# Optimization experiments

Hardware: AMD Instinct MI355X
Metric: run time of the kernel (lower is better)

The kernel has to match this reference:

```python
import jax, jax.numpy as jnp
import numpy as np
from jax.scipy.special import gammaln

# NQ_IN + 4 == 2*H is required because the two kernel=1, padding=1 convs grow the
# length axis by 4 and the following nn.Linear(2H, H) acts on the length axis.
B, NQ_IN, NK, QDIM, KDIM, H = 16, 2044, 1024, 80, 256, 1024


def setup_inputs() -> dict:
    ks = jax.random.split(jax.random.key(0), 14)
    s = 0.02
    return {
        "query": jax.random.normal(ks[0], (B, NQ_IN, QDIM), jnp.float32),
        "key": jax.random.normal(ks[1], (B, NK, KDIM), jnp.float32),
        "query_lens": jnp.full((B,), 2 * H, jnp.int32),
        "key_lens": jnp.full((B,), NK, jnp.int32),
        # query branch params (Conv1d k=1 stored as (out,in); Linear as (out,in))
        "qc1_w": jax.random.normal(ks[2], (2 * H, QDIM), jnp.float32) * s,
        "qc1_b": jax.random.normal(ks[3], (2 * H,), jnp.float32) * s,
        "qc2_w": jax.random.normal(ks[4], (2 * H, 2 * H), jnp.float32) * s,
        "qc2_b": jax.random.normal(ks[5], (2 * H,), jnp.float32) * s,
        "ql_w": jax.random.normal(ks[6], (H, 2 * H), jnp.float32) * s,
        "ql_b": jax.random.normal(ks[7], (H,), jnp.float32) * s,
        # key branch params
        "kc_w": jax.random.normal(ks[8], (H, KDIM, 3), jnp.float32) * s,
        "kc_b": jax.random.normal(ks[9], (H,), jnp.float32) * s,
        "kl1_w": jax.random.normal(ks[10], (2 * H, H), jnp.float32) * s,
        "kl1_b": jax.random.normal(ks[11], (2 * H,), jnp.float32) * s,
        "kl2_w": jax.random.normal(ks[12], (H, 2 * H), jnp.float32) * s,
        "kl2_b": jax.random.normal(ks[13], (H,), jnp.float32) * s,
    }


def _log_beta_binom(query_lens, key_lens, tq, tk):
    # Standard MAS beta-binomial alignment prior over a (tq, tk) grid.
    i = jnp.arange(tq, dtype=jnp.float32)[None, :, None]
    j = jnp.arange(tk, dtype=jnp.float32)[None, None, :]
    ql = query_lens.astype(jnp.float32)[:, None, None]
    kl = key_lens.astype(jnp.float32)[:, None, None]
    a = i + 1.0
    b = jnp.maximum(ql - i, 1.0)
    n = jnp.maximum(kl - 1.0, 0.0)
    nmj = jnp.maximum(n - j, 0.0)

    def betaln(x, y):
        return gammaln(x) + gammaln(y) - gammaln(x + y)

    logp = (gammaln(n + 1.0) - gammaln(j + 1.0) - gammaln(nmj + 1.0)
            + betaln(j + a, nmj + b) - betaln(a, b))
    valid = (i < ql) & (j < kl)
    return jnp.where(valid, logp, -1e9)


def _forward(query, key, query_lens, key_lens,
             qc1_w, qc1_b, qc2_w, qc2_b, ql_w, ql_b,
             kc_w, kc_b, kl1_w, kl1_b, kl2_w, kl2_b):
    # query branch: b n c -> b c n, two k=1/p=1 convs (pad length, pointwise), Linear over LENGTH axis
    q = jnp.transpose(query, (0, 2, 1))                       # (B, QDIM, NQ_IN)
    q = jnp.pad(q, ((0, 0), (0, 0), (1, 1)))
    q = jnp.einsum('bcn,oc->bon', q, qc1_w) + qc1_b[None, :, None]   # (B, 2H, NQ_IN+2)
    q = jnp.pad(q, ((0, 0), (0, 0), (1, 1)))
    q = jnp.einsum('bcn,oc->bon', q, qc2_w) + qc2_b[None, :, None]   # (B, 2H, 2H)
    q = jnp.einsum('bcn,hn->bch', q, ql_w) + ql_b                    # (B, 2H, H) Linear on length axis

    # key branch: b n c -> b c n, Conv1d k=3 p=1, then two Linears over LENGTH axis
    k = jnp.transpose(key, (0, 2, 1))                         # (B, KDIM, NK)
    k = jax.lax.conv_general_dilated(k, kc_w, (1,), ((1, 1),),
                                     dimension_numbers=('NCH', 'OIH', 'NCH'))
    k = k + kc_b[None, :, None]                               # (B, H, NK=H)
    k = jnp.einsum('bcn,on->bco', k, kl1_w) + kl1_b           # (B, H, 2H)
    k = jnp.einsum('bco,ho->bch', k, kl2_w) + kl2_b           # (B, H, H)

    # dist = -cdist(q, k), computed via the GEMM form (same as torch.cdist mm mode)
    sq = (jnp.sum(q * q, -1)[:, :, None] + jnp.sum(k * k, -1)[:, None, :]
          - 2.0 * jnp.einsum('bnd,bmd->bnm', q, k))           # (B, 2H, H)
    dist = -jnp.sqrt(jnp.maximum(sq, 1e-12))

    prior = _log_beta_binom(query_lens, key_lens, q.shape[1], k.shape[1])
    return jax.nn.log_softmax(dist + prior, axis=-1)


def reference(query, key, query_lens, key_lens,
              qc1_w, qc1_b, qc2_w, qc2_b, ql_w, ql_b,
              kc_w, kc_b, kl1_w, kl1_b, kl2_w, kl2_b):
    return _forward(query, key, query_lens, key_lens,
                    qc1_w, qc1_b, qc2_w, qc2_b, ql_w, ql_b,
                    kc_w, kc_b, kl1_w, kl1_b, kl2_w, kl2_b)
```

## Files before the change

### kernel.cpp

```cpp
#include <hip/hip_runtime.h>
#include <math.h>

typedef unsigned short u16;
typedef float floatx4 __attribute__((ext_vector_type(4)));
typedef __bf16 bf16x8 __attribute__((ext_vector_type(8)));

#define BB   16
#define TQ   2048
#define TK   1024
#define HH   1024
#define H2   2048
#define QD   80
#define QDP  128
#define KD   256
#define NQ   2044
#define NKEY 1024

__device__ __forceinline__ u16 f2bf(float f) {
  unsigned int u = __float_as_uint(f);
  u = u + 0x7fffu + ((u >> 16) & 1u);
  return (u16)(u >> 16);
}
__device__ __forceinline__ float bf2f(u16 s) {
  return __uint_as_float(((unsigned int)s) << 16);
}

__global__ __launch_bounds__(256) void prep_all_k(
    const float* __restrict__ qc2_w, const float* __restrict__ kl2_w,
    const float* __restrict__ ql_w, const float* __restrict__ kc_w,
    const float* __restrict__ kl1_w,
    u16* __restrict__ qc2w, u16* __restrict__ kl2w, u16* __restrict__ qlw2,
    u16* __restrict__ kcp, float* __restrict__ colsum1, float* __restrict__ tbl)
{
  long b = blockIdx.x;
  const int t = threadIdx.x;
  __shared__ float red[256];
  if (b < 16384) {
    long i = b * 256 + t; qc2w[i] = f2bf(qc2_w[i]); return;
  }
  b -= 16384;
  if (b < 8192) {
    long i = b * 256 + t; kl2w[i] = f2bf(kl2_w[i]); return;
  }
  b -= 8192;
  if (b < 8192) {
    long i = b * 256 + t;
    int n = (int)(i & 2047);
    int h = (int)(i >> 11);
    qlw2[i] = (n < NQ) ? f2bf(ql_w[(long)h * H2 + n + 2]) : (u16)0; return;
  }
  b -= 8192;
  if (b < 3072) {
    long i = b * 256 + t;
    int r = (int)(i % 768);
    int o = (int)(i / 768);
    int tt = r >> 8, d = r & 255;
    kcp[i] = f2bf(kc_w[((long)o * KD + d) * 3 + tt]); return;
  }
  b -= 3072;
  if (b < 2048) {
    const float* row = kl1_w + b * (long)HH;
    float s = row[t] + row[t + 256] + row[t + 512] + row[t + 768];
    red[t] = s; __syncthreads();
    for (int st = 128; st > 0; st >>= 1) { if (t < st) red[t] += red[t + st]; __syncthreads(); }
    if (!t) colsum1[b] = red[0];
    return;
  }
  b -= 2048;
  { int i = (int)(b * 256 + t); if (i < 8192) tbl[i] = i ? (float)lgamma((double)i) : 0.0f; }
}

__global__ __launch_bounds__(256) void tpack_k(
    const float* __restrict__ kl1_w, const float* __restrict__ qc1_w,
    const float* __restrict__ query,
    u16* __restrict__ kl1T, u16* __restrict__ qc1T, u16* __restrict__ qT)
{
  __shared__ float tile[64][65];
  int bid = blockIdx.x;
  const int tid = threadIdx.x;
  const int r4 = tid >> 6, c = tid & 63;
  const float* src; u16* dst;
  int sr0, sc0, srcR, srcC, srcStride, dstC;
  if (bid < 512) {
    sr0 = (bid >> 4) * 64; sc0 = (bid & 15) * 64;
    src = kl1_w; srcR = 2048; srcC = 1024; srcStride = 1024;
    dst = kl1T; dstC = 2048;
  } else if ((bid -= 512) < 64) {
    sr0 = (bid >> 1) * 64; sc0 = (bid & 1) * 64;
    src = qc1_w; srcR = 2048; srcC = QD; srcStride = QD;
    dst = qc1T; dstC = 2048;
  } else {
    bid -= 64;
    const int b16 = bid >> 6, r = bid & 63;
    sr0 = (r >> 1) * 64; sc0 = (r & 1) * 64;
    src = query + (long)b16 * NQ * QD; srcR = NQ; srcC = QD; srcStride = QD;
    dst = qT + (long)b16 * QDP * 2048; dstC = 2048;
  }
#pragma unroll
  for (int rr = r4; rr < 64; rr += 4) {
    const int gr = sr0 + rr, gc = sc0 + c;
    tile[rr][c] = (gr < srcR && gc < srcC) ? src[(long)gr * srcStride + gc] : 0.f;
  }
  __syncthreads();
#pragma unroll
  for (int rr = r4; rr < 64; rr += 4)
    dst[(long)(sc0 + rr) * dstC + sr0 + c] = f2bf(tile[c][rr]);
}

__global__ __launch_bounds__(256) void pack_kcolT_k(const float* __restrict__ key, u16* __restrict__ out) {
  __shared__ float tile[64][65];
  const int bid = blockIdx.x, tid = threadIdx.x;
  const int b = bid >> 6, r = bid & 63;
  const int m0 = (r >> 2) * 64;
  const int d0 = (r & 3) * 64;
  const int r4 = tid >> 6, c = tid & 63;
#pragma unroll
  for (int rr = r4; rr < 64; rr += 4)
    tile[rr][c] = key[((long)b * NKEY + m0 + rr) * KD + d0 + c];
  __syncthreads();
#pragma unroll
  for (int t = 0; t < 3; t++) {
    const int n = m0 + 1 - t + c;
    if (n >= 0 && n < NKEY) {
#pragma unroll
      for (int rr = r4; rr < 64; rr += 4)
        out[((long)b * 768 + t * 256 + d0 + rr) * NKEY + n] = f2bf(tile[c][rr]);
    }
  }
  if (m0 == 0 && c == 0) {
#pragma unroll
    for (int rr = r4; rr < 64; rr += 4)
      out[((long)b * 768 + d0 + rr) * NKEY + 0] = (u16)0;
  }
  if (m0 == 960 && c == 0) {
#pragma unroll
    for (int rr = r4; rr < 64; rr += 4)
      out[((long)b * 768 + 512 + d0 + rr) * NKEY + (NKEY - 1)] = (u16)0;
  }
}

__global__ __launch_bounds__(256) void fold_bias_k(
    const float* __restrict__ qc2_w, const float* __restrict__ qc1_b, const float* __restrict__ qc2_b,
    const float* __restrict__ kl2_w, const float* __restrict__ kl1_b, const float* __restrict__ kl2_b,
    const float* __restrict__ ql_w, const float* __restrict__ colsum1,
    float* __restrict__ bqm, float* __restrict__ bkv, float* __restrict__ s1v, float* __restrict__ s0v,
    float* __restrict__ wsum)
{
  const int bid = blockIdx.x, t = threadIdx.x;
  float s = 0.f, s2 = 0.f;
  if (bid < H2) {
    const float* row = qc2_w + (long)bid * H2;
    for (int k = t; k < H2; k += 256) s += row[k] * qc1_b[k];
  } else if (bid < H2 + HH) {
    const float* row = kl2_w + (long)(bid - H2) * H2;
    for (int k = t; k < H2; k += 256) { const float rv = row[k]; s += rv * kl1_b[k]; s2 += rv * colsum1[k]; }
  } else {
    const float* row = ql_w + (long)(bid - H2 - HH) * H2;
    for (int m = 1 + t; m <= H2 - 2; m += 256) s += row[m];
  }
  __shared__ float red[256];
  __shared__ float red2[256];
  red[t] = s; red2[t] = s2; __syncthreads();
  for (int st = 128; st > 0; st >>= 1) {
    if (t < st) { red[t] += red[t + st]; red2[t] += red2[t + st]; }
    __syncthreads();
  }
  if (!t) {
    if (bid < H2) bqm[bid] = red[0] + qc2_b[bid];
    else if (bid < H2 + HH) { bkv[bid - H2] = red[0] + kl2_b[bid - H2]; wsum[bid - H2] = red2[0]; }
    else {
      int h = bid - H2 - HH;
      s1v[h] = red[0];
      s0v[h] = ql_w[(long)h * H2] + ql_w[(long)h * H2 + H2 - 1];
    }
  }
}

__device__ __forceinline__ void gld_lds16(const u16* g, u16* l) {
  __builtin_amdgcn_global_load_lds((const __attribute__((address_space(1))) void*)g,
                                   (__attribute__((address_space(3))) void*)l, 16, 0, 0);
}

template<int OUTF32>
__global__ __launch_bounds__(256) void gemm_bt(
    const u16* __restrict__ A, const u16* __restrict__ B, void* __restrict__ Cv,
    int M, int N, int K, int lda, int ldb, int swap, int kspl,
    long sA, long sB, long sC, long sN,
    const float* __restrict__ colb, const float* __restrict__ rowb,
    const float* __restrict__ r1m, const float* __restrict__ r1n,
    const float* __restrict__ r2m, const float* __restrict__ r2n)
{
  __shared__ __align__(16) u16 As[128 * 32];
  __shared__ __align__(16) u16 Bs[128 * 32];
  const int bz = blockIdx.z;
  const int bb_ = (kspl > 1) ? bz / kspl : bz;
  const int ks_ = (kspl > 1) ? bz - bb_ * kspl : 0;
  const int tid  = threadIdx.x;
  const int lane = tid & 63;
  const int wv = tid >> 6;
  const int wm = ((tid >> 7) & 1) * 64;
  const int wn = ((tid >> 6) & 1) * 64;
  const int m0 = (swap ? blockIdx.x : blockIdx.y) * 128;
  const int n0 = (swap ? blockIdx.y : blockIdx.x) * 128;

  const int srow = wv * 32 + (lane >> 2);
  const int scol = (lane & 3) << 3;
  const u16* ga = A + bb_ * sA + (long)ks_ * K + (long)(m0 + srow) * lda + scol;
  const u16* gb = B + bb_ * sB + (long)ks_ * K + (long)(n0 + srow) * ldb + scol;
  u16* la0 = &As[(wv * 32) * 32];
  u16* la1 = &As[(wv * 32 + 16) * 32];
  u16* lb0 = &Bs[(wv * 32) * 32];
  u16* lb1 = &Bs[(wv * 32 + 16) * 32];
  const long a16 = (long)16 * lda;
  const long b16 = (long)16 * ldb;

  floatx4 acc[4][4];
#pragma unroll
  for (int a_ = 0; a_ < 4; a_++)
#pragma unroll
    for (int b_ = 0; b_ < 4; b_++) acc[a_][b_] = (floatx4){0.f, 0.f, 0.f, 0.f};

  const int fr = lane & 15;
  const int fk = (lane >> 4) << 3;

  for (int kb = 0; kb < K; kb += 32) {
    gld_lds16(ga,       la0);
    gld_lds16(ga + a16, la1);
    gld_lds16(gb,       lb0);
    gld_lds16(gb + b16, lb1);
    ga += 32; gb += 32;
    __syncthreads();
    bf16x8 af[4], bfr[4];
#pragma unroll
    for (int mi = 0; mi < 4; mi++)
      af[mi] = *reinterpret_cast<const bf16x8*>(&As[(wm + mi * 16 + fr) * 32 + fk]);
#pragma unroll
    for (int ni = 0; ni < 4; ni++)
      bfr[ni] = *reinterpret_cast<const bf16x8*>(&Bs[(wn + ni * 16 + fr) * 32 + fk]);
#pragma unroll
    for (int mi = 0; mi < 4; mi++)
#pragma unroll
      for (int ni = 0; ni < 4; ni++)
        acc[mi][ni] = __builtin_amdgcn_mfma_f32_16x16x32_bf16(af[mi], bfr[ni], acc[mi][ni], 0, 0, 0);
    __syncthreads();
  }

  const int fr4 = (lane >> 4) << 2;
  const int fc  = lane & 15;
  u16*   Cb16 = (u16*)Cv + (long)bz * sC;
  float* Cb32 = (float*)Cv + (long)bz * sC;
  const float* cbp  = colb ? colb + (long)bb_ * sN : nullptr;
  const float* r1np = r1n ? r1n + (long)bb_ * sN : nullptr;
  const float* r2np = r2n ? r2n + (long)bb_ * sN : nullptr;
#pragma unroll
  for (int mi = 0; mi < 4; mi++) {
#pragma unroll
    for (int ni = 0; ni < 4; ni++) {
      const int gm0 = m0 + wm + mi * 16 + fr4;
      const int gn  = n0 + wn + ni * 16 + fc;
      const float cbv  = cbp ? cbp[gn] : 0.f;
      const float r1nv = r1np ? r1np[gn] : 0.f;
      const float r2nv = r2np ? r2np[gn] : 0.f;
#pragma unroll
      for (int rr = 0; rr < 4; rr++) {
        const int gm = gm0 + rr;
        float v = acc[mi][ni][rr] + cbv;
        if (rowb) v += rowb[gm];
        if (r1m)  v += r1m[gm] * r1nv;
        if (r2m)  v += r2m[gm] * r2nv;
        if (OUTF32) Cb32[(long)gm * N + gn] = v;
        else        Cb16[(long)gm * N + gn] = f2bf(v);
      }
    }
  }
}

__global__ __launch_bounds__(256) void reduce_bk_k(const float* __restrict__ P, u16* __restrict__ out,
                                                   long chunk, int S, long total) {
  long j = ((long)blockIdx.x * 256 + threadIdx.x) * 4;
  if (j >= total) return;
  long b = j / chunk;
  const float* p = P + j + b * chunk * (S - 1);
  float4 s = *reinterpret_cast<const float4*>(p);
  for (int t = 1; t < S; t++) {
    const float4 v = *reinterpret_cast<const float4*>(p + (long)t * chunk);
    s.x += v.x; s.y += v.y; s.z += v.z; s.w += v.w;
  }
  union { u16 h[4]; uint2 u; } o;
  o.h[0] = f2bf(s.x); o.h[1] = f2bf(s.y); o.h[2] = f2bf(s.z); o.h[3] = f2bf(s.w);
  *reinterpret_cast<uint2*>(out + j) = o.u;
}

__global__ __launch_bounds__(256) void u_k(
    const u16* __restrict__ TpT, const float* __restrict__ qlb,
    const float* __restrict__ s1, const float* __restrict__ s0,
    const float* __restrict__ tbl, const int* __restrict__ klens,
    float* __restrict__ u0, float* __restrict__ u1, float* __restrict__ u2,
    float* __restrict__ sc, float* __restrict__ c1)
{
  const int bid = blockIdx.x, t = threadIdx.x;
  __shared__ float4 red[256];
  if (bid < BB * QDP) {
    uint2 v = reinterpret_cast<const uint2*>(TpT + (long)bid * HH)[t];
    float a0 = bf2f((u16)(v.x & 0xffff)), a1 = bf2f((u16)(v.x >> 16));
    float a2 = bf2f((u16)(v.y & 0xffff)), a3 = bf2f((u16)(v.y >> 16));
    float4 q  = reinterpret_cast<const float4*>(qlb)[t];
    float4 w1 = reinterpret_cast<const float4*>(s1)[t];
    float4 w0 = reinterpret_cast<const float4*>(s0)[t];
    float4 s;
    s.x = a0 * q.x  + a1 * q.y  + a2 * q.z  + a3 * q.w;
    s.y = a0 * w1.x + a1 * w1.y + a2 * w1.z + a3 * w1.w;
    s.z = a0 * w0.x + a1 * w0.y + a2 * w0.z + a3 * w0.w;
    s.w = 0.f;
    red[t] = s; __syncthreads();
    for (int st = 128; st > 0; st >>= 1) {
      if (t < st) { red[t].x += red[t + st].x; red[t].y += red[t + st].y; red[t].z += red[t + st].z; }
      __syncthreads();
    }
    if (!t) { u0[bid] = red[0].x; u1[bid] = red[0].y; u2[bid] = red[0].z; }
  } else if (bid < BB * QDP + 6) {
    const int idx = bid - BB * QDP;
    const float* X = (idx == 1 || idx == 5) ? s1 : (idx == 2) ? s0 : qlb;
    const float* Y = (idx == 1 || idx == 3) ? s1 : (idx == 0) ? qlb : s0;
    float4 x = reinterpret_cast<const float4*>(X)[t];
    float4 y = reinterpret_cast<const float4*>(Y)[t];
    float4 s; s.x = x.x * y.x + x.y * y.y + x.z * y.z + x.w * y.w; s.y = s.z = s.w = 0.f;
    red[t] = s; __syncthreads();
    for (int st = 128; st > 0; st >>= 1) {
      if (t < st) red[t].x += red[t + st].x;
      __syncthreads();
    }
    if (!t) sc[idx] = red[0].x;
  } else {
    const int idx = bid - (BB * QDP + 6);
    const int b = idx >> 2;
    const int j = ((idx & 3) << 8) | t;
    const int kl = klens[b];
    const int n_ = (kl - 1 > 0) ? kl - 1 : 0;
    int x1 = j + 1; if (x1 > 8191) x1 = 8191;
    int x2 = n_ - j + 1; if (x2 < 0) x2 = 0; if (x2 > 8191) x2 = 8191;
    c1[b * TK + j] = tbl[x1] + tbl[x2];
  }
}

__global__ __launch_bounds__(256) void qn_k(
    const u16* __restrict__ Wq, const float* __restrict__ WqG,
    const float* __restrict__ u0, const float* __restrict__ u1, const float* __restrict__ u2,
    const float* __restrict__ bqm, const float* __restrict__ qc2_b,
    const float* __restrict__ sc, float* __restrict__ qn)
{
  const int bx = blockIdx.x, t = threadIdx.x;
  const int b = bx >> 10;
  const int i = ((bx & 1023) << 1) | (t >> 7);
  const int d = t & 127;
  const float w  = bf2f(Wq[(long)i * QDP + d]);
  const float g  = WqG[((long)b * H2 + i) * QDP + d];
  const float bq = bqm[i], q2 = qc2_b[i];
  const float uu = u0[b * QDP + d] + bq * u1[b * QDP + d] + q2 * u2[b * QDP + d];
  __shared__ float red[256];
  red[t] = w * (g + 2.f * uu); __syncthreads();
  for (int s = 64; s > 0; s >>= 1) { if ((t & 127) < s) red[t] += red[t + s]; __syncthreads(); }
  if (d == 0) {
    const float cst = sc[0] + bq * bq * sc[1] + q2 * q2 * sc[2]
                    + 2.f * (bq * sc[3] + q2 * sc[4] + bq * q2 * sc[5]);
    qn[b * TQ + i] = red[t] + cst;
  }
}

__global__ __launch_bounds__(256) void rownormk_k(
    const u16* __restrict__ K3, const float* __restrict__ qlb,
    const float* __restrict__ s1, const float* __restrict__ s0,
    float* __restrict__ kn, float* __restrict__ yb, float* __restrict__ y1, float* __restrict__ y0)
{
  const long r = blockIdx.x;
  const int t = threadIdx.x;
  uint2 v = reinterpret_cast<const uint2*>(K3 + r * HH)[t];
  float a0 = bf2f((u16)(v.x & 0xffff)), a1 = bf2f((u16)(v.x >> 16));
  float a2 = bf2f((u16)(v.y & 0xffff)), a3 = bf2f((u16)(v.y >> 16));
  float4 q  = reinterpret_cast<const float4*>(qlb)[t];
  float4 w1 = reinterpret_cast<const float4*>(s1)[t];
  float4 w0 = reinterpret_cast<const float4*>(s0)[t];
  float4 s;
  s.x = a0 * a0   + a1 * a1   + a2 * a2   + a3 * a3;
  s.y = a0 * q.x  + a1 * q.y  + a2 * q.z  + a3 * q.w;
  s.z = a0 * w1.x + a1 * w1.y + a2 * w1.z + a3 * w1.w;
  s.w = a0 * w0.x + a1 * w0.y + a2 * w0.z + a3 * w0.w;
  __shared__ float4 red[256];
  red[t] = s; __syncthreads();
  for (int st = 128; st > 0; st >>= 1) {
    if (t < st) {
      red[t].x += red[t + st].x; red[t].y += red[t + st].y;
      red[t].z += red[t + st].z; red[t].w += red[t + st].w;
    }
    __syncthreads();
  }
  if (!t) { kn[r] = red[0].x; yb[r] = red[0].y; y1[r] = red[0].z; y0[r] = red[0].w; }
}

__global__ __launch_bounds__(256) void finalize_k(
    const u16* __restrict__ S, const float* __restrict__ qn, const float* __restrict__ kn,
    const float* __restrict__ c1,
    const int* __restrict__ qlens, const int* __restrict__ klens,
    const float* __restrict__ tbl, float* __restrict__ out)
{
  const int i = blockIdx.x;
  const int b = blockIdx.y;
  const int tid = threadIdx.x;
  const long rowoff = ((long)b * TQ + i) * TK;
  const int ql = qlens[b], kl = klens[b];
  const int n_ = (kl - 1 > 0) ? kl - 1 : 0;
  const int bb = (ql - i > 1) ? ql - i : 1;
  const float qni = qn[b * TQ + i];
#define TG(x) tbl[((x) < 8191) ? (x) : 8191]
  const float CrowR = TG(n_ + 1) + TG(i + 1 + bb) - TG(i + 1) - TG(bb) - TG(i + 1 + n_ + bb);
  const bool ivalid = (i < ql);
  const int j0 = tid << 2;
  const float4 kn4 = *reinterpret_cast<const float4*>(kn + b * TK + j0);
  const float4 c14 = *reinterpret_cast<const float4*>(c1 + b * TK + j0);
  const uint2 sv = *reinterpret_cast<const uint2*>(S + rowoff + j0);
  const float knl[4] = {kn4.x, kn4.y, kn4.z, kn4.w};
  const float c1l[4] = {c14.x, c14.y, c14.z, c14.w};
  const u16 sl[4] = {(u16)(sv.x & 0xffff), (u16)(sv.x >> 16), (u16)(sv.y & 0xffff), (u16)(sv.y >> 16)};

  float v[4];
  float lmax = -3.4e38f;
#pragma unroll
  for (int l = 0; l < 4; l++) {
    const int j = j0 + l;
    const float sq = fmaxf(qni + knl[l] - 2.0f * bf2f(sl[l]), 1e-12f);
    const float dist = -sqrtf(sq);
    float lp;
    if (ivalid && j < kl) {
      lp = CrowR - c1l[l] + TG(i + j + 1) + TG(n_ - j + bb);
    } else {
      lp = -1e9f;
    }
    v[l] = dist + lp;
    lmax = fmaxf(lmax, v[l]);
  }
  __shared__ float red[256];
  red[tid] = lmax; __syncthreads();
  for (int s = 128; s > 0; s >>= 1) { if (tid < s) red[tid] = fmaxf(red[tid], red[tid + s]); __syncthreads(); }
  const float gmax = red[0]; __syncthreads();
  float lsum = 0.f;
#pragma unroll
  for (int l = 0; l < 4; l++) lsum += expf(v[l] - gmax);
  red[tid] = lsum; __syncthreads();
  for (int s = 128; s > 0; s >>= 1) { if (tid < s) red[tid] += red[tid + s]; __syncthreads(); }
  const float lse = gmax + logf(red[0]);
  const float4 o4 = {v[0] - lse, v[1] - lse, v[2] - lse, v[3] - lse};
  *reinterpret_cast<float4*>(out + rowoff + j0) = o4;
#undef TG
}

extern "C" void kernel_launch(void* const* d_in, const int* in_sizes, int n_in,
                              void* d_out, int out_size, void* d_ws, size_t ws_size,
                              hipStream_t stream)
{
  (void)in_sizes; (void)n_in; (void)out_size; (void)ws_size;
  const float* query = (const float*)d_in[0];
  const float* key   = (const float*)d_in[1];
  const int*   qlens = (const int*)d_in[2];
  const int*   klens = (const int*)d_in[3];
  const float* qc1_w = (const float*)d_in[4];
  const float* qc1_b = (const float*)d_in[5];
  const float* qc2_w = (const float*)d_in[6];
  const float* qc2_b = (const float*)d_in[7];
  const float* ql_w  = (const float*)d_in[8];
  const float* ql_b  = (const float*)d_in[9];
  const float* kc_w  = (const float*)d_in[10];
  const float* kc_b  = (const float*)d_in[11];
  const float* kl1_w = (const float*)d_in[12];
  const float* kl1_b = (const float*)d_in[13];
  const float* kl2_w = (const float*)d_in[14];
  const float* kl2_b = (const float*)d_in[15];

  size_t off = 0;
  char* ws = (char*)d_ws;
  auto alloc = [&](size_t bytes) -> char* {
    char* p = ws + off; off += (bytes + 255) & ~(size_t)255; return p;
  };
  u16* qc2w_bf = (u16*)alloc(2ull * H2 * H2);
  u16* qc1T_bf = (u16*)alloc(2ull * QDP * H2);
  u16* kl2w_bf = (u16*)alloc(2ull * HH * H2);
  u16* kl1T_bf = (u16*)alloc(2ull * HH * H2);
  u16* qT_bf   = (u16*)alloc(2ull * BB * QDP * 2048);
  u16* kcolT_bf= (u16*)d_ws;
  u16* S_bf    = (u16*)d_ws;
  u16* qlw2_bf = (u16*)alloc(2ull * HH * 2048);
  u16* kcp_bf  = (u16*)alloc(2ull * HH * 768);
  u16* TpT_bf  = (u16*)alloc(2ull * H2 * HH);
  char* pool   = alloc(2ull * BB * HH * NKEY);
  float* Pbuf  = (float*)pool;
  u16* X_bf    = (u16*)pool;
  float* tbl  = (float*)alloc(4ull * 8192);
  u16* Wq_bf  = (u16*)alloc(2ull * H2 * QDP);
  u16* Wk_bf  = (u16*)alloc(2ull * HH * NKEY);
  float* bqm  = (float*)alloc(4ull * H2);
  float* bkv  = (float*)alloc(4ull * HH);
  float* s1v  = (float*)alloc(4ull * HH);
  float* s0v  = (float*)alloc(4ull * HH);
  float* wsum = (float*)alloc(4ull * HH);
  float* colsum1 = (float*)alloc(4ull * H2);
  u16* K3_bf  = (u16*)alloc(2ull * BB * TK * HH);
  float* qnv  = (float*)alloc(4ull * BB * TQ);
  float* knv  = (float*)alloc(4ull * BB * TK);
  float* ybv  = (float*)alloc(4ull * BB * TK);
  float* y1v  = (float*)alloc(4ull * BB * TK);
  float* y0v  = (float*)alloc(4ull * BB * TK);
  float* u0v  = (float*)alloc(4ull * BB * QDP);
  float* u1v  = (float*)alloc(4ull * BB * QDP);
  float* u2v  = (float*)alloc(4ull * BB * QDP);
  float* c1v  = (float*)alloc(4ull * BB * TK);
  float* scv  = (float*)alloc(256);
  float* WqG  = (float*)d_out;
  u16* G_bf   = (u16*)((char*)d_out + 16777216);
  u16* Z2_bf  = (u16*)((char*)d_out + 16777216 + 524288);

  prep_all_k<<<37920, 256, 0, stream>>>(qc2_w, kl2_w, ql_w, kc_w, kl1_w,
                                        qc2w_bf, kl2w_bf, qlw2_bf, kcp_bf, colsum1, tbl);
  tpack_k<<<1600, 256, 0, stream>>>(kl1_w, qc1_w, query, kl1T_bf, qc1T_bf, qT_bf);
  fold_bias_k<<<4096, 256, 0, stream>>>(qc2_w, qc1_b, qc2_b, kl2_w, kl1_b, kl2_b, ql_w, colsum1,
                                        bqm, bkv, s1v, s0v, wsum);

  gemm_bt<1><<<dim3(1, 16, 16), 256, 0, stream>>>(qc2w_bf, qc1T_bf, Pbuf, H2, QDP, 128,
      H2, H2, 0, 16, 0, 0, (long)H2 * QDP, 0,
      nullptr, nullptr, nullptr, nullptr, nullptr, nullptr);
  reduce_bk_k<<<256, 256, 0, stream>>>(Pbuf, Wq_bf, (long)H2 * QDP, 16, (long)H2 * QDP);

  gemm_bt<1><<<dim3(8, 8, 8), 256, 0, stream>>>(kl2w_bf, kl1T_bf, Pbuf, HH, NKEY, 256,
      H2, H2, 0, 8, 0, 0, (long)HH * NKEY, 0,
      nullptr, nullptr, nullptr, nullptr, nullptr, nullptr);
  reduce_bk_k<<<1024, 256, 0, stream>>>(Pbuf, Wk_bf, (long)HH * NKEY, 8, (long)HH * NKEY);

  gemm_bt<1><<<dim3(8, 16, 4), 256, 0, stream>>>(qT_bf, qlw2_bf, Pbuf, H2, HH, 512,
      2048, 2048, 0, 4, 0, 0, (long)H2 * HH, 0,
      nullptr, nullptr, nullptr, nullptr, nullptr, nullptr);
  reduce_bk_k<<<2048, 256, 0, stream>>>(Pbuf, TpT_bf, (long)H2 * HH, 4, (long)H2 * HH);

  gemm_bt<1><<<dim3(1, 1, 128), 256, 0, stream>>>(TpT_bf, TpT_bf, Pbuf, 128, 128, 128,
      HH, HH, 0, 8, (long)QDP * HH, (long)QDP * HH, 128 * 128, 0,
      nullptr, nullptr, nullptr, nullptr, nullptr, nullptr);
  reduce_bk_k<<<256, 256, 0, stream>>>(Pbuf, G_bf, 128 * 128, 8, (long)BB * 128 * 128);

  gemm_bt<1><<<dim3(1, 16, 16), 256, 0, stream>>>(Wq_bf, G_bf, WqG, H2, QDP, QDP,
      QDP, QDP, 0, 1, 0, (long)QDP * QDP, (long)H2 * QDP, 0,
      nullptr, nullptr, nullptr, nullptr, nullptr, nullptr);
  u_k<<<BB * QDP + 6 + 64, 256, 0, stream>>>(TpT_bf, ql_b, s1v, s0v, tbl, klens,
                                             u0v, u1v, u2v, scv, c1v);
  qn_k<<<BB * TQ / 2, 256, 0, stream>>>(Wq_bf, WqG, u0v, u1v, u2v, bqm, qc2_b, scv, qnv);

  pack_kcolT_k<<<1024, 256, 0, stream>>>(key, kcolT_bf);
  gemm_bt<0><<<dim3(6, 8, BB), 256, 0, stream>>>(Wk_bf, kcolT_bf, X_bf, HH, 768, NKEY,
      NKEY, NKEY, 0, 1, 0, (long)768 * NKEY, (long)HH * 768, 0,
      nullptr, nullptr, nullptr, nullptr, nullptr, nullptr);
  gemm_bt<0><<<dim3(8, 8, BB), 256, 0, stream>>>(kcp_bf, X_bf, K3_bf, HH, NKEY, 768,
      768, 768, 1, 1, 0, (long)HH * 768, (long)TK * HH, 0,
      bkv, nullptr, kc_b, wsum, nullptr, nullptr);

  gemm_bt<1><<<dim3(8, 1, 32), 256, 0, stream>>>(K3_bf, TpT_bf, Pbuf, TK, QDP, 512,
      HH, HH, 1, 2, (long)TK * HH, (long)QDP * HH, (long)TK * QDP, 0,
      nullptr, nullptr, nullptr, nullptr, nullptr, nullptr);
  reduce_bk_k<<<2048, 256, 0, stream>>>(Pbuf, Z2_bf, (long)TK * QDP, 2, (long)BB * TK * QDP);

  rownormk_k<<<BB * TK, 256, 0, stream>>>(K3_bf, ql_b, s1v, s0v, knv, ybv, y1v, y0v);

  gemm_bt<0><<<dim3(8, 16, BB), 256, 0, stream>>>(Wq_bf, Z2_bf, S_bf, H2, TK, QDP,
      QDP, QDP, 0, 1, 0, (long)TK * QDP, (long)TQ * TK, (long)TK,
      ybv, nullptr, bqm, y1v, qc2_b, y0v);

  finalize_k<<<dim3(TQ, BB, 1), 256, 0, stream>>>(S_bf, qnv, knv, c1v, qlens, klens, tbl, (float*)d_out);
}
```

Baseline: 656.1 us.

## Fuse distance and prior into final GEMM epilogue, simplify softmax kernel

The last GEMM's epilogue now computes sqrt distance, validity masking and the beta-binomial prior, and writes fp32 logits straight to the output buffer. The prior is factored into per-row, per-column and per-(i+j) tables built in u_k. Finalize becomes an in-place log-softmax that uses wavefront shuffles and exp2. This drops the bf16 S intermediate and the gathered table lookups from the finalize pass, at the cost of an fp32 read and write of the full output. Scores are no longer rounded to bf16 before the softmax, which changes numerics slightly.

```diff
diff --git a/kernel.cpp b/kernel.cpp
--- a/kernel.cpp
+++ b/kernel.cpp
@@ -15,6 +15,7 @@
 #define KD   256
 #define NQ   2044
 #define NKEY 1024
+#define T12N 3072
 
 __device__ __forceinline__ u16 f2bf(float f) {
   unsigned int u = __float_as_uint(f);
@@ -23,6 +24,9 @@
 }
 __device__ __forceinline__ float bf2f(u16 s) {
   return __uint_as_float(((unsigned int)s) << 16);
+}
+__device__ __forceinline__ float tgf(const float* __restrict__ tbl, int x) {
+  return tbl[(x < 8191) ? (x < 0 ? 0 : x) : 8191];
 }
 
 __global__ __launch_bounds__(256) void prep_all_k(
@@ -181,14 +185,18 @@
                                    (__attribute__((address_space(3))) void*)l, 16, 0, 0);
 }
 
-template<int OUTF32>
+template<int MODE>
 __global__ __launch_bounds__(256) void gemm_bt(
     const u16* __restrict__ A, const u16* __restrict__ B, void* __restrict__ Cv,
     int M, int N, int K, int lda, int ldb, int swap, int kspl,
     long sA, long sB, long sC, long sN,
     const float* __restrict__ colb, const float* __restrict__ rowb,
     const float* __restrict__ r1m, const float* __restrict__ r1n,
-    const float* __restrict__ r2m, const float* __restrict__ r2n)
+    const float* __restrict__ r2m, const float* __restrict__ r2n,
+    const float* __restrict__ c1p, const float* __restrict__ qnp,
+    const float* __restrict__ knp, const float* __restrict__ crowp,
+    const float* __restrict__ t12p,
+    const int* __restrict__ qlensp, const int* __restrict__ klensp)
 {
   __shared__ __align__(16) u16 As[128 * 32];
   __shared__ __align__(16) u16 Bs[128 * 32];
@@ -252,6 +260,8 @@
   const float* cbp  = colb ? colb + (long)bb_ * sN : nullptr;
   const float* r1np = r1n ? r1n + (long)bb_ * sN : nullptr;
   const float* r2np = r2n ? r2n + (long)bb_ * sN : nullptr;
+  int qlv = 0, klv = 0;
+  if (MODE == 2) { qlv = qlensp[bb_]; klv = klensp[bb_]; }
 #pragma unroll
   for (int mi = 0; mi < 4; mi++) {
 #pragma unroll
@@ -261,6 +271,14 @@
       const float cbv  = cbp ? cbp[gn] : 0.f;
       const float r1nv = r1np ? r1np[gn] : 0.f;
       const float r2nv = r2np ? r2np[gn] : 0.f;
+      float knj = 0.f, c1j = 0.f;
+      union { float4 v4; float a[4]; } qn4, cr4;
+      if (MODE == 2) {
+        knj = knp[(long)bb_ * TK + gn];
+        c1j = c1p[(long)bb_ * TK + gn];
+        qn4.v4 = *reinterpret_cast<const float4*>(qnp + (long)bb_ * TQ + gm0);
+        cr4.v4 = *reinterpret_cast<const float4*>(crowp + (long)bb_ * TQ + gm0);
+      }
 #pragma unroll
       for (int rr = 0; rr < 4; rr++) {
         const int gm = gm0 + rr;
@@ -268,8 +286,16 @@
         if (rowb) v += rowb[gm];
         if (r1m)  v += r1m[gm] * r1nv;
         if (r2m)  v += r2m[gm] * r2nv;
-        if (OUTF32) Cb32[(long)gm * N + gn] = v;
-        else        Cb16[(long)gm * N + gn] = f2bf(v);
+        if (MODE == 2) {
+          const float sq = fmaxf(qn4.a[rr] + knj - 2.0f * v, 1e-12f);
+          const float dist = -sqrtf(sq);
+          float res = -1e9f;
+          if (gm < qlv && gn < klv)
+            res = dist + cr4.a[rr] - c1j + t12p[(long)bb_ * T12N + gm + gn];
+          Cb32[(long)gm * N + gn] = res;
+        }
+        else if (MODE == 1) Cb32[(long)gm * N + gn] = v;
+        else                Cb16[(long)gm * N + gn] = f2bf(v);
       }
     }
   }
@@ -294,9 +320,10 @@
 __global__ __launch_bounds__(256) void u_k(
     const u16* __restrict__ TpT, const float* __restrict__ qlb,
     const float* __restrict__ s1, const float* __restrict__ s0,
-    const float* __restrict__ tbl, const int* __restrict__ klens,
+    const float* __restrict__ tbl, const int* __restrict__ qlens, const int* __restrict__ klens,
     float* __restrict__ u0, float* __restrict__ u1, float* __restrict__ u2,
-    float* __restrict__ sc, float* __restrict__ c1)
+    float* __restrict__ sc, float* __restrict__ c1,
+    float* __restrict__ crow, float* __restrict__ t12)
 {
   const int bid = blockIdx.x, t = threadIdx.x;
   __shared__ float4 red[256];
@@ -331,15 +358,29 @@
       __syncthreads();
     }
     if (!t) sc[idx] = red[0].x;
-  } else {
+  } else if (bid < BB * QDP + 6 + 64) {
     const int idx = bid - (BB * QDP + 6);
     const int b = idx >> 2;
     const int j = ((idx & 3) << 8) | t;
     const int kl = klens[b];
     const int n_ = (kl - 1 > 0) ? kl - 1 : 0;
-    int x1 = j + 1; if (x1 > 8191) x1 = 8191;
-    int x2 = n_ - j + 1; if (x2 < 0) x2 = 0; if (x2 > 8191) x2 = 8191;
-    c1[b * TK + j] = tbl[x1] + tbl[x2];
+    c1[b * TK + j] = tgf(tbl, j + 1) + tgf(tbl, n_ - j + 1);
+  } else if (bid < BB * QDP + 6 + 64 + 128) {
+    const int idx = bid - (BB * QDP + 6 + 64);
+    const int b = idx >> 3;
+    const int i = ((idx & 7) << 8) | t;
+    const int ql = qlens[b], kl = klens[b];
+    const int n_ = (kl - 1 > 0) ? kl - 1 : 0;
+    const int bb = (ql - i > 1) ? ql - i : 1;
+    crow[b * TQ + i] = tgf(tbl, n_ + 1) + tgf(tbl, i + 1 + bb) - tgf(tbl, i + 1)
+                     - tgf(tbl, bb) - tgf(tbl, i + 1 + n_ + bb);
+  } else {
+    const int idx = bid - (BB * QDP + 6 + 64 + 128);
+    const int b = idx / 12;
+    const int s = (idx - b * 12) * 256 + t;
+    const int ql = qlens[b], kl = klens[b];
+    const int n_ = (kl - 1 > 0) ? kl - 1 : 0;
+    t12[b * T12N + s] = tgf(tbl, s + 1) + tgf(tbl, n_ + ql - s);
   }
 }
 
@@ -397,60 +438,31 @@
   if (!t) { kn[r] = red[0].x; yb[r] = red[0].y; y1[r] = red[0].z; y0[r] = red[0].w; }
 }
 
-__global__ __launch_bounds__(256) void finalize_k(
-    const u16* __restrict__ S, const float* __restrict__ qn, const float* __restrict__ kn,
-    const float* __restrict__ c1,
-    const int* __restrict__ qlens, const int* __restrict__ klens,
-    const float* __restrict__ tbl, float* __restrict__ out)
+__global__ __launch_bounds__(256) void finalize_k(float* __restrict__ out)
 {
   const int i = blockIdx.x;
   const int b = blockIdx.y;
   const int tid = threadIdx.x;
   const long rowoff = ((long)b * TQ + i) * TK;
-  const int ql = qlens[b], kl = klens[b];
-  const int n_ = (kl - 1 > 0) ? kl - 1 : 0;
-  const int bb = (ql - i > 1) ? ql - i : 1;
-  const float qni = qn[b * TQ + i];
-#define TG(x) tbl[((x) < 8191) ? (x) : 8191]
-  const float CrowR = TG(n_ + 1) + TG(i + 1 + bb) - TG(i + 1) - TG(bb) - TG(i + 1 + n_ + bb);
-  const bool ivalid = (i < ql);
-  const int j0 = tid << 2;
-  const float4 kn4 = *reinterpret_cast<const float4*>(kn + b * TK + j0);
-  const float4 c14 = *reinterpret_cast<const float4*>(c1 + b * TK + j0);
-  const uint2 sv = *reinterpret_cast<const uint2*>(S + rowoff + j0);
-  const float knl[4] = {kn4.x, kn4.y, kn4.z, kn4.w};
-  const float c1l[4] = {c14.x, c14.y, c14.z, c14.w};
-  const u16 sl[4] = {(u16)(sv.x & 0xffff), (u16)(sv.x >> 16), (u16)(sv.y & 0xffff), (u16)(sv.y >> 16)};
-
-  float v[4];
-  float lmax = -3.4e38f;
-#pragma unroll
-  for (int l = 0; l < 4; l++) {
-    const int j = j0 + l;
-    const float sq = fmaxf(qni + knl[l] - 2.0f * bf2f(sl[l]), 1e-12f);
-    const float dist = -sqrtf(sq);
-    float lp;
-    if (ivalid && j < kl) {
-      lp = CrowR - c1l[l] + TG(i + j + 1) + TG(n_ - j + bb);
-    } else {
-      lp = -1e9f;
-    }
-    v[l] = dist + lp;
-    lmax = fmaxf(lmax, v[l]);
-  }
-  __shared__ float red[256];
-  red[tid] = lmax; __syncthreads();
-  for (int s = 128; s > 0; s >>= 1) { if (tid < s) red[tid] = fmaxf(red[tid], red[tid + s]); __syncthreads(); }
-  const float gmax = red[0]; __syncthreads();
-  float lsum = 0.f;
-#pragma unroll
-  for (int l = 0; l < 4; l++) lsum += expf(v[l] - gmax);
-  red[tid] = lsum; __syncthreads();
-  for (int s = 128; s > 0; s >>= 1) { if (tid < s) red[tid] += red[tid + s]; __syncthreads(); }
-  const float lse = gmax + logf(red[0]);
-  const float4 o4 = {v[0] - lse, v[1] - lse, v[2] - lse, v[3] - lse};
-  *reinterpret_cast<float4*>(out + rowoff + j0) = o4;
-#undef TG
+  float4 v = *reinterpret_cast<const float4*>(out + rowoff + (tid << 2));
+  float m = fmaxf(fmaxf(v.x, v.y), fmaxf(v.z, v.w));
+#pragma unroll
+  for (int k = 1; k < 64; k <<= 1) m = fmaxf(m, __shfl_xor(m, k, 64));
+  __shared__ float wred[8];
+  if ((tid & 63) == 0) wred[tid >> 6] = m;
+  __syncthreads();
+  const float gmax = fmaxf(fmaxf(wred[0], wred[1]), fmaxf(wred[2], wred[3]));
+  const float L2E = 1.4426950408889634f;
+  float ls = exp2f((v.x - gmax) * L2E) + exp2f((v.y - gmax) * L2E)
+           + exp2f((v.z - gmax) * L2E) + exp2f((v.w - gmax) * L2E);
+#pragma unroll
+  for (int k = 1; k < 64; k <<= 1) ls += __shfl_xor(ls, k, 64);
+  if ((tid & 63) == 0) wred[4 + (tid >> 6)] = ls;
+  __syncthreads();
+  const float tot = (wred[4] + wred[5]) + (wred[6] + wred[7]);
+  const float lse = gmax + logf(tot);
+  v.x -= lse; v.y -= lse; v.z -= lse; v.w -= lse;
+  *reinterpret_cast<float4*>(out + rowoff + (tid << 2)) = v;
 }
 
 extern "C" void kernel_launch(void* const* d_in, const int* in_sizes, int n_in,
@@ -486,7 +498,7 @@
   u16* kl1T_bf = (u16*)alloc(2ull * HH * H2);
   u16* qT_bf   = (u16*)alloc(2ull * BB * QDP * 2048);
   u16* kcolT_bf= (u16*)d_ws;
-  u16* S_bf    = (u16*)d_ws;
+  u16* Z2_bf   = (u16*)d_ws;
   u16* qlw2_bf = (u16*)alloc(2ull * HH * 2048);
   u16* kcp_bf  = (u16*)alloc(2ull * HH * 768);
   u16* TpT_bf  = (u16*)alloc(2ull * H2 * HH);
@@ -512,10 +524,11 @@
   float* u1v  = (float*)alloc(4ull * BB * QDP);
   float* u2v  = (float*)alloc(4ull * BB * QDP);
   float* c1v  = (float*)alloc(4ull * BB * TK);
+  float* crowv= (float*)alloc(4ull * BB * TQ);
+  float* t12v = (float*)alloc(4ull * BB * T12N);
   float* scv  = (float*)alloc(256);
   float* WqG  = (float*)d_out;
   u16* G_bf   = (u16*)((char*)d_out + 16777216);
-  u16* Z2_bf  = (u16*)((char*)d_out + 16777216 + 524288);
 
   prep_all_k<<<37920, 256, 0, stream>>>(qc2_w, kl2_w, ql_w, kc_w, kl1_w,
                                         qc2w_bf, kl2w_bf, qlw2_bf, kcp_bf, colsum1, tbl);
@@ -525,49 +538,58 @@
 
   gemm_bt<1><<<dim3(1, 16, 16), 256, 0, stream>>>(qc2w_bf, qc1T_bf, Pbuf, H2, QDP, 128,
       H2, H2, 0, 16, 0, 0, (long)H2 * QDP, 0,
-      nullptr, nullptr, nullptr, nullptr, nullptr, nullptr);
+      nullptr, nullptr, nullptr, nullptr, nullptr, nullptr,
+      nullptr, nullptr, nullptr, nullptr, nullptr, nullptr, nullptr);
   reduce_bk_k<<<256, 256, 0, stream>>>(Pbuf, Wq_bf, (long)H2 * QDP, 16, (long)H2 * QDP);
 
   gemm_bt<1><<<dim3(8, 8, 8), 256, 0, stream>>>(kl2w_bf, kl1T_bf, Pbuf, HH, NKEY, 256,
       H2, H2, 0, 8, 0, 0, (long)HH * NKEY, 0,
-      nullptr, nullptr, nullptr, nullptr, nullptr, nullptr);
+      nullptr, nullptr, nullptr, nullptr, nullptr, nullptr,
+      nullptr, nullptr, nullptr, nullptr, nullptr, nullptr, nullptr);
   reduce_bk_k<<<1024, 256, 0, stream>>>(Pbuf, Wk_bf, (long)HH * NKEY, 8, (long)HH * NKEY);
 
   gemm_bt<1><<<dim3(8, 16, 4), 256, 0, stream>>>(qT_bf, qlw2_bf, Pbuf, H2, HH, 512,
       2048, 2048, 0, 4, 0, 0, (long)H2 * HH, 0,
-      nullptr, nullptr, nullptr, nullptr, nullptr, nullptr);
+      nullptr, nullptr, nullptr, nullptr, nullptr, nullptr,
+      nullptr, nullptr, nullptr, nullptr, nullptr, nullptr, nullptr);
   reduce_bk_k<<<2048, 256, 0, stream>>>(Pbuf, TpT_bf, (long)H2 * HH, 4, (long)H2 * HH);
 
   gemm_bt<1><<<dim3(1, 1, 128), 256, 0, stream>>>(TpT_bf, TpT_bf, Pbuf, 128, 128, 128,
       HH, HH, 0, 8, (long)QDP * HH, (long)QDP * HH, 128 * 128, 0,
-      nullptr, nullptr, nullptr, nullptr, nullptr, nullptr);
+      nullptr, nullptr, nullptr, nullptr, nullptr, nullptr,
+      nullptr, nullptr, nullptr, nullptr, nullptr, nullptr, nullptr);
   reduce_bk_k<<<256, 256, 0, stream>>>(Pbuf, G_bf, 128 * 128, 8, (long)BB * 128 * 128);
 
   gemm_bt<1><<<dim3(1, 16, 16), 256, 0, stream>>>(Wq_bf, G_bf, WqG, H2, QDP, QDP,
       QDP, QDP, 0, 1, 0, (long)QDP * QDP, (long)H2 * QDP, 0,
-      nullptr, nullptr, nullptr, nullptr, nullptr, nullptr);
-  u_k<<<BB * QDP + 6 + 64, 256, 0, stream>>>(TpT_bf, ql_b, s1v, s0v, tbl, klens,
-                                             u0v, u1v, u2v, scv, c1v);
+      nullptr, nullptr, nullptr, nullptr, nullptr, nullptr,
+      nullptr, nullptr, nullptr, nullptr, nullptr, nullptr, nullptr);
+  u_k<<<BB * QDP + 6 + 64 + 128 + 192, 256, 0, stream>>>(TpT_bf, ql_b, s1v, s0v, tbl, qlens, klens,
+                                                         u0v, u1v, u2v, scv, c1v, crowv, t12v);
   qn_k<<<BB * TQ / 2, 256, 0, stream>>>(Wq_bf, WqG, u0v, u1v, u2v, bqm, qc2_b, scv, qnv);
 
   pack_kcolT_k<<<1024, 256, 0, stream>>>(key, kcolT_bf);
   gemm_bt<0><<<dim3(6, 8, BB), 256, 0, stream>>>(Wk_bf, kcolT_bf, X_bf, HH, 768, NKEY,
       NKEY, NKEY, 0, 1, 0, (long)768 * NKEY, (long)HH * 768, 0,
-      nullptr, nullptr, nullptr, nullptr, nullptr, nullptr);
+      nullptr, nullptr, nullptr, nullptr, nullptr, nullptr,
+      nullptr, nullptr, nullptr, nullptr, nullptr, nullptr, nullptr);
   gemm_bt<0><<<dim3(8, 8, BB), 256, 0, stream>>>(kcp_bf, X_bf, K3_bf, HH, NKEY, 768,
       768, 768, 1, 1, 0, (long)HH * 768, (long)TK * HH, 0,
-      bkv, nullptr, kc_b, wsum, nullptr, nullptr);
+      bkv, nullptr, kc_b, wsum, nullptr, nullptr,
+      nullptr, nullptr, nullptr, nullptr, nullptr, nullptr, nullptr);
 
   gemm_bt<1><<<dim3(8, 1, 32), 256, 0, stream>>>(K3_bf, TpT_bf, Pbuf, TK, QDP, 512,
       HH, HH, 1, 2, (long)TK * HH, (long)QDP * HH, (long)TK * QDP, 0,
-      nullptr, nullptr, nullptr, nullptr, nullptr, nullptr);
+      nullptr, nullptr, nullptr, nullptr, nullptr, nullptr,
+      nullptr, nullptr, nullptr, nullptr, nullptr, nullptr, nullptr);
   reduce_bk_k<<<2048, 256, 0, stream>>>(Pbuf, Z2_bf, (long)TK * QDP, 2, (long)BB * TK * QDP);
 
   rownormk_k<<<BB * TK, 256, 0, stream>>>(K3_bf, ql_b, s1v, s0v, knv, ybv, y1v, y0v);
 
-  gemm_bt<0><<<dim3(8, 16, BB), 256, 0, stream>>>(Wq_bf, Z2_bf, S_bf, H2, TK, QDP,
+  gemm_bt<2><<<dim3(8, 16, BB), 256, 0, stream>>>(Wq_bf, Z2_bf, (float*)d_out, H2, TK, QDP,
       QDP, QDP, 0, 1, 0, (long)TK * QDP, (long)TQ * TK, (long)TK,
-      ybv, nullptr, bqm, y1v, qc2_b, y0v);
-
-  finalize_k<<<dim3(TQ, BB, 1), 256, 0, stream>>>(S_bf, qnv, knv, c1v, qlens, klens, tbl, (float*)d_out);
-}
+      ybv, nullptr, bqm, y1v, qc2_b, y0v,
+      c1v, qnv, knv, crowv, t12v, qlens, klens);
+
+  finalize_k<<<dim3(TQ, BB, 1), 256, 0, stream>>>((float*)d_out);
+}
```

Result: no change. 650.9 us (-0.8%).
